# Performance work log

Measured on AMD Instinct MI355X. Metric: run time of the kernel, lower is better.

## Reference

```python
import jax, jax.numpy as jnp
import numpy as np

B, L, F, E, D, N_OUT, FC = 2048, 100, 64, 256, 256, 3, 128


def _lstm_cell(x, h, c, Wi, Wh, b):
    gates = x @ Wi + h @ Wh + b  # (B, 4H)
    i, f, g, o = jnp.split(gates, 4, axis=-1)
    c_new = jax.nn.sigmoid(f) * c + jax.nn.sigmoid(i) * jnp.tanh(g)
    h_new = jax.nn.sigmoid(o) * jnp.tanh(c_new)
    return h_new, c_new


def setup_inputs() -> dict:
    key = jax.random.key(0)
    ks = jax.random.split(key, 12)
    s = 0.05
    return {
        "x": jax.random.normal(ks[0], (B, L, F), jnp.float32),
        # encoder input-attention (shared across timesteps, as in [layer]*look_back)
        "Wa": jax.random.normal(ks[1], (F + E, F), jnp.float32) * s,
        "ba": jnp.zeros((F,), jnp.float32),
        # encoder LSTM cell
        "Wi": jax.random.normal(ks[2], (F, 4 * E), jnp.float32) * s,
        "Wh": jax.random.normal(ks[3], (E, 4 * E), jnp.float32) * s,
        "be": jnp.zeros((4 * E,), jnp.float32),
        # decoder temporal attention
        "Wd": jax.random.normal(ks[4], (E + D, D), jnp.float32) * s,
        "bd": jnp.zeros((D,), jnp.float32),
        "Wl": jax.random.normal(ks[5], (D, 1), jnp.float32) * s,
        "bl": jnp.zeros((1,), jnp.float32),
        # decoder LSTM cell
        "Wdi": jax.random.normal(ks[6], (E, 4 * D), jnp.float32) * s,
        "Wdh": jax.random.normal(ks[7], (D, 4 * D), jnp.float32) * s,
        "bdec": jnp.zeros((4 * D,), jnp.float32),
        # output head: tanh(D->FC) then tanh(FC->1)
        "Wf": jax.random.normal(ks[8], (D, FC), jnp.float32) * s,
        "bf": jnp.zeros((FC,), jnp.float32),
        "Wo": jax.random.normal(ks[9], (FC, 1), jnp.float32) * s,
        "bo": jnp.zeros((1,), jnp.float32),
    }


def reference(x, Wa, ba, Wi, Wh, be, Wd, bd, Wl, bl, Wdi, Wdh, bdec, Wf, bf, Wo, bo):
    # ---------- encoder: per-timestep input attention + LSTM cell ----------
    x_t = jnp.transpose(x, (1, 0, 2))  # (L, B, F)

    def enc_step(carry, xt):
        h, c = carry
        energies = jnp.tanh(jnp.concatenate([xt, h], axis=1) @ Wa + ba)  # (B, F)
        a = jax.nn.softmax(energies, axis=1)
        enc_in = a * xt  # attended input (B, F)
        h, c = _lstm_cell(enc_in, h, c, Wi, Wh, be)
        return (h, c), h

    h0 = jnp.zeros((B, E), x.dtype)
    c0 = jnp.zeros((B, E), x.dtype)
    _, enc_out = jax.lax.scan(enc_step, (h0, c0), x_t)  # (L, B, E)

    # ---------- decoder: temporal attention over encoder states + LSTM ----------
    h_d = jnp.zeros((B, D), x.dtype)
    c_d = jnp.zeros((B, D), x.dtype)
    outs = []
    for _ in range(N_OUT):  # small fixed output horizon
        con = jnp.broadcast_to(h_d[None, :, :], (L, B, D))
        en = jnp.tanh(jnp.concatenate([enc_out, con], axis=2) @ Wd + bd)  # (L, B, D)
        scores = en @ Wl + bl  # (L, B, 1)
        alpha = jax.nn.softmax(scores, axis=0)  # over time
        ctx = jnp.sum(alpha * enc_out, axis=0)  # (B, E)
        h_d, c_d = _lstm_cell(ctx, h_d, c_d, Wdi, Wdh, bdec)
        fc = jnp.tanh(h_d @ Wf + bf)  # (B, FC)
        outs.append(jnp.tanh(fc @ Wo + bo))  # (B, 1)
    return jnp.concatenate(outs, axis=1)  # (B, n_output)
```

## Files before the change

kernel.cpp:

```cpp
#include <hip/hip_runtime.h>
#include <math.h>

#define BB 2048
#define LL 100
#define FF 64
#define EE 256
#define DD 256
#define NOUT 3

#define COMP(v, i) ((i) == 0 ? (v).x : (i) == 1 ? (v).y : (i) == 2 ? (v).z : (v).w)

typedef unsigned short u16;
typedef unsigned int u32;
typedef __attribute__((ext_vector_type(8))) __bf16 bf16x8;
typedef __attribute__((ext_vector_type(4))) float f32x4;
typedef __attribute__((ext_vector_type(2))) float f32x2;

#define MFMA_(A, B, C) __builtin_amdgcn_mfma_f32_16x16x32_bf16((A), (B), (C), 0, 0, 0)

__device__ __forceinline__ float sigmoidf_(float x) {
    return 1.0f / (1.0f + expf(-x));
}
__device__ __forceinline__ float tanhf_(float x) {
    return 1.0f - 2.0f / (1.0f + expf(2.0f * x));
}
__device__ __forceinline__ u16 f2b_(float f) {
    u32 u = __float_as_uint(f);
    u = (u + 0x7FFFu + ((u >> 16) & 1u)) >> 16;
    return (u16)u;
}
__device__ __forceinline__ float b2f_(u16 b) {
    return __uint_as_float(((u32)b) << 16);
}
__device__ __forceinline__ u32 pack2_(float a, float b) {
    return (u32)f2b_(a) | ((u32)f2b_(b) << 16);
}
__device__ __forceinline__ f32x4 splat4(float b) {
    f32x4 v; v[0] = b; v[1] = b; v[2] = b; v[3] = b; return v;
}
__device__ __forceinline__ void split8(const float* v, uint4& H, uint4& L) {
    u16 h[8], lo[8];
    #pragma unroll
    for (int e = 0; e < 8; ++e) {
        h[e]  = f2b_(v[e]);
        lo[e] = f2b_(v[e] - b2f_(h[e]));
    }
    H = make_uint4((u32)h[0]  | ((u32)h[1]  << 16), (u32)h[2]  | ((u32)h[3]  << 16),
                   (u32)h[4]  | ((u32)h[5]  << 16), (u32)h[6]  | ((u32)h[7]  << 16));
    L = make_uint4((u32)lo[0] | ((u32)lo[1] << 16), (u32)lo[2] | ((u32)lo[3] << 16),
                   (u32)lo[4] | ((u32)lo[5] << 16), (u32)lo[6] | ((u32)lo[7] << 16));
}

#define AF(mt, kt, p, ln) (((((mt) * 10 + (kt)) * 2 + (p)) * 64 + (ln)) * 8)

__global__ __launch_bounds__(64) void w_prep(
    const float* __restrict__ Wi, const float* __restrict__ Wh,
    const float* __restrict__ Wa, u16* __restrict__ wp)
{
    const int bid = blockIdx.x;
    const int l   = threadIdx.x;
    const int isA = (bid >= 640);
    const int b2  = isA ? bid - 640 : bid;
    const int nt  = b2 / 10, kt = b2 - nt * 10;
    const int col = nt * 16 + (l & 15);

    float v[8];
    #pragma unroll
    for (int e = 0; e < 8; ++e) {
        const int k = kt * 32 + ((l >> 4) << 3) + e;
        v[e] = isA ? Wa[(size_t)k * 64 + col]
                   : (k < 64 ? Wi[(size_t)k * 1024 + col]
                             : Wh[(size_t)(k - 64) * 1024 + col]);
    }
    uint4 H, L;
    split8(v, H, L);
    *(uint4*)&wp[(size_t)bid * 1024 + (size_t)l * 8]       = H;
    *(uint4*)&wp[(size_t)bid * 1024 + 512 + (size_t)l * 8] = L;
}

__global__ __launch_bounds__(1024) void enc_mfma4(
    const float* __restrict__ x,
    const float* __restrict__ ba, const float* __restrict__ be,
    const u16* __restrict__ wp,
    float* __restrict__ enc_out,
    float* __restrict__ hbuf,
    u32* __restrict__ flags)
{
    __shared__ u16   aFrag[20480];
    __shared__ float x_s[32 * 68];
    __shared__ float e_s[32 * 68];
    __shared__ float gate_s[4][32][64];

    const int bid = blockIdx.x;
    const int g   = (bid & 7) | ((bid >> 5) << 3);
    const int p   = (bid >> 3) & 3;
    const int row0 = g * 32;
    const int tid = threadIdx.x;
    const int l   = tid & 63;
    const int w   = tid >> 6;

    for (int v = tid; v < 20480 / 2; v += 1024) ((u32*)aFrag)[v] = 0u;

    const int ntW = (w >> 2) * 16 + p * 4 + (w & 3);
    uint4 BhR[10];
    #pragma unroll
    for (int kt = 0; kt < 10; ++kt)
        BhR[kt] = *(const uint4*)&wp[(size_t)(ntW * 10 + kt) * 1024 + (size_t)l * 8];

    const float be_r = be[(size_t)ntW * 16 + (l & 15)];
    const float ba_r = (w < 8) ? ba[(w & 3) * 16 + (l & 15)] : 0.f;

    float c_state[2] = {0.f, 0.f};

    __syncthreads();

    for (int t = 0; t < LL; ++t) {
        if (t > 0) {
            if (tid == 0) {
                const u32 target = 4u * (u32)t;
                int guard = 0;
                while (__hip_atomic_load(&flags[g], __ATOMIC_RELAXED,
                                         __HIP_MEMORY_SCOPE_AGENT) < target) {
                    __builtin_amdgcn_s_sleep(1);
                    if (++guard > 2000000) break;
                }
            }
            __syncthreads();
        }

        if (tid < 256) {
            const int kt2 = tid >> 7;
            const int mt  = (tid >> 6) & 1;
            const int l2  = tid & 63;
            const int row2 = mt * 16 + (l2 & 15);
            const int f0   = kt2 * 32 + ((l2 >> 4) << 3);
            const float* xp = x + (size_t)(row0 + row2) * (LL * FF) + (size_t)t * FF + f0;
            float4 xa = *(const float4*)xp;
            float4 xb = *(const float4*)(xp + 4);
            float v[8] = {xa.x, xa.y, xa.z, xa.w, xb.x, xb.y, xb.z, xb.w};
            uint4 H, L;
            split8(v, H, L);
            *(uint4*)&aFrag[AF(mt, kt2, 0, l2)] = H;
            *(uint4*)&aFrag[AF(mt, kt2, 1, l2)] = L;
            *(float4*)&x_s[row2 * 68 + f0]     = xa;
            *(float4*)&x_s[row2 * 68 + f0 + 4] = xb;
        } else if (t > 0) {
            const int v   = tid - 256;
            const int prl = v >> 8;
            const int vv  = v & 255;
            const int row = vv >> 3;
            const int i8  = vv & 7;
            const int ugp = (p + 1 + prl) & 3;
            const int u8  = ugp * 64 + i8 * 8;
            const float* hp_g = hbuf + ((size_t)((t - 1) & 1) * BB + row0 + row) * 256 + u8;
            f32x4 a4, b4;
            asm volatile("global_load_dwordx4 %0, %2, off sc0 sc1\n\t"
                         "global_load_dwordx4 %1, %3, off sc0 sc1\n\t"
                         "s_waitcnt vmcnt(0)"
                         : "=v"(a4), "=v"(b4)
                         : "v"(hp_g), "v"(hp_g + 4) : "memory");
            float v8[8] = {a4[0], a4[1], a4[2], a4[3], b4[0], b4[1], b4[2], b4[3]};
            uint4 H, L;
            split8(v8, H, L);
            const int mt = row >> 4, rowT = row & 15;
            const int kt_h = 2 + (u8 >> 5);
            const int g2   = (u8 & 31) >> 3;
            const int ln   = rowT + (g2 << 4);
            *(uint4*)&aFrag[AF(mt, kt_h, 0, ln)] = H;
            *(uint4*)&aFrag[AF(mt, kt_h, 1, ln)] = L;
        }
        __syncthreads();

        if (w < 8) {
            const int mt  = w >> 2;
            const int nta = w & 3;
            f32x4 ea = splat4(ba_r);
            #pragma unroll
            for (int kt = 0; kt < 10; ++kt) {
                bf16x8 Ah = *(const bf16x8*)&aFrag[AF(mt, kt, 0, l)];
                bf16x8 Al = *(const bf16x8*)&aFrag[AF(mt, kt, 1, l)];
                const size_t o = (size_t)(640 + nta * 10 + kt) * 1024 + (size_t)l * 8;
                bf16x8 Bh = *(const bf16x8*)&wp[o];
                bf16x8 Bl = *(const bf16x8*)&wp[o + 512];
                ea = MFMA_(Ah, Bh, ea);
                ea = MFMA_(Al, Bh, ea);
                ea = MFMA_(Ah, Bl, ea);
            }
            const int colA = nta * 16 + (l & 15);
            #pragma unroll
            for (int r = 0; r < 4; ++r) {
                const int rowT = ((l >> 4) << 2) + r;
                e_s[(mt * 16 + rowT) * 68 + colA] = tanhf_(ea[r]);
            }
        }
        __syncthreads();

        if (tid < 512) {
            const int row2 = tid >> 4;
            const int c4   = (tid & 15) * 4;
            float4 ev = *(const float4*)&e_s[row2 * 68 + c4];
            float m = fmaxf(fmaxf(ev.x, ev.y), fmaxf(ev.z, ev.w));
            #pragma unroll
            for (int msk = 8; msk >= 1; msk >>= 1) m = fmaxf(m, __shfl_xor(m, msk, 64));
            float4 ex;
            ex.x = expf(ev.x - m); ex.y = expf(ev.y - m);
            ex.z = expf(ev.z - m); ex.w = expf(ev.w - m);
            float s = ex.x + ex.y + ex.z + ex.w;
            #pragma unroll
            for (int msk = 8; msk >= 1; msk >>= 1) s += __shfl_xor(s, msk, 64);
            const float inv = 1.f / s;
            float4 xv = *(const float4*)&x_s[row2 * 68 + c4];
            float ein[4] = { ex.x * inv * xv.x, ex.y * inv * xv.y,
                             ex.z * inv * xv.z, ex.w * inv * xv.w };
            const int mt   = row2 >> 4;
            const int rowT = row2 & 15;
            const int kt   = c4 >> 5;
            const int g2   = (c4 & 31) >> 3;
            const int e0   = c4 & 7;
            const int ln   = rowT + (g2 << 4);
            ushort4 h4, l4;
            #pragma unroll
            for (int e = 0; e < 4; ++e) {
                u16 hh = f2b_(ein[e]);
                u16 ll = f2b_(ein[e] - b2f_(hh));
                if (e == 0) { h4.x = hh; l4.x = ll; } else if (e == 1) { h4.y = hh; l4.y = ll; }
                else if (e == 2) { h4.z = hh; l4.z = ll; } else { h4.w = hh; l4.w = ll; }
            }
            *(ushort4*)&aFrag[AF(mt, kt, 0, ln) + e0] = h4;
            *(ushort4*)&aFrag[AF(mt, kt, 1, ln) + e0] = l4;
        }
        __syncthreads();

        f32x4 acc0 = splat4(be_r), acc1 = splat4(be_r);
        #pragma unroll
        for (int kt = 0; kt < 10; ++kt) {
            bf16x8 Ah0 = *(const bf16x8*)&aFrag[AF(0, kt, 0, l)];
            bf16x8 Al0 = *(const bf16x8*)&aFrag[AF(0, kt, 1, l)];
            bf16x8 Ah1 = *(const bf16x8*)&aFrag[AF(1, kt, 0, l)];
            bf16x8 Al1 = *(const bf16x8*)&aFrag[AF(1, kt, 1, l)];
            bf16x8 Bl  = *(const bf16x8*)&wp[(size_t)(ntW * 10 + kt) * 1024 + 512 + (size_t)l * 8];
            bf16x8 Bh  = __builtin_bit_cast(bf16x8, BhR[kt]);
            acc0 = MFMA_(Ah0, Bh, acc0);
            acc1 = MFMA_(Ah1, Bh, acc1);
            acc0 = MFMA_(Al0, Bh, acc0);
            acc1 = MFMA_(Al1, Bh, acc1);
            acc0 = MFMA_(Ah0, Bl, acc0);
            acc1 = MFMA_(Ah1, Bl, acc1);
        }
        {
            const int gate = w >> 2;
            const int ulb  = (w & 3) * 16 + (l & 15);
            #pragma unroll
            for (int r = 0; r < 4; ++r) {
                const int rT = ((l >> 4) << 2) + r;
                gate_s[gate][rT][ulb]      = acc0[r];
                gate_s[gate][16 + rT][ulb] = acc1[r];
            }
        }
        __syncthreads();

        {
            const int row = tid >> 5;
            const int q2  = (tid & 31) * 2;
            float gi0 = gate_s[0][row][q2], gi1 = gate_s[0][row][q2 + 1];
            float gf0 = gate_s[1][row][q2], gf1 = gate_s[1][row][q2 + 1];
            float gg0 = gate_s[2][row][q2], gg1 = gate_s[2][row][q2 + 1];
            float go0 = gate_s[3][row][q2], go1 = gate_s[3][row][q2 + 1];
            float cv0 = sigmoidf_(gf0) * c_state[0] + sigmoidf_(gi0) * tanhf_(gg0);
            float cv1 = sigmoidf_(gf1) * c_state[1] + sigmoidf_(gi1) * tanhf_(gg1);
            c_state[0] = cv0; c_state[1] = cv1;
            float hv0 = sigmoidf_(go0) * tanhf_(cv0);
            float hv1 = sigmoidf_(go1) * tanhf_(cv1);
            const int u_g = p * 64 + q2;
            *(float2*)&enc_out[((size_t)t * BB + row0 + row) * 256 + u_g]
                = make_float2(hv0, hv1);
            float* hp_g = hbuf + ((size_t)(t & 1) * BB + row0 + row) * 256 + u_g;
            f32x2 hv2; hv2[0] = hv0; hv2[1] = hv1;
            asm volatile("global_store_dwordx2 %0, %1, off sc0 sc1"
                         :: "v"(hp_g), "v"(hv2) : "memory");
            const int mt = row >> 4, rowT = row & 15;
            const int kt_h = 2 + (u_g >> 5);
            const int g2   = (u_g & 31) >> 3;
            const int ln   = rowT + (g2 << 4);
            const int e    = u_g & 7;
            ((u32*)aFrag)[(AF(mt, kt_h, 0, ln) + e) >> 1] = pack2_(hv0, hv1);
            u16 h0 = f2b_(hv0), h1 = f2b_(hv1);
            ((u32*)aFrag)[(AF(mt, kt_h, 1, ln) + e) >> 1] =
                (u32)f2b_(hv0 - b2f_(h0)) | ((u32)f2b_(hv1 - b2f_(h1)) << 16);
        }
        asm volatile("s_waitcnt vmcnt(0)" ::: "memory");
        __syncthreads();
        if (tid == 0)
            __hip_atomic_fetch_add(&flags[g], 1u, __ATOMIC_RELEASE,
                                   __HIP_MEMORY_SCOPE_AGENT);
    }
}

__global__ __launch_bounds__(256) void gemm_nk256(
    const float* __restrict__ A, const float* __restrict__ W,
    const float* __restrict__ bias, float* __restrict__ C, int skip_gemm)
{
    __shared__ float a_s[32 * 256];
    const int m0   = blockIdx.x * 32;
    const int tid  = threadIdx.x;
    const int lane = tid & 63;
    const int rg   = tid >> 6;
    const int n0   = lane * 4;

    float4 bias4 = make_float4(0.f, 0.f, 0.f, 0.f);
    if (bias) bias4 = *(const float4*)&bias[n0];

    if (skip_gemm) {
        #pragma unroll
        for (int r = 0; r < 8; ++r)
            *(float4*)&C[(size_t)(m0 + rg * 8 + r) * 256 + n0] = bias4;
        return;
    }

    for (int v = tid; v < 32 * 64; v += 256)
        ((float4*)a_s)[v] = ((const float4*)(A + (size_t)m0 * 256))[v];
    __syncthreads();

    float4 acc[8];
    #pragma unroll
    for (int r = 0; r < 8; ++r) acc[r] = bias4;

    #pragma unroll 2
    for (int k = 0; k < 256; k += 4) {
        float4 wv[4];
        #pragma unroll
        for (int kk = 0; kk < 4; ++kk)
            wv[kk] = *(const float4*)&W[(size_t)(k + kk) * 256 + n0];
        float4 av[8];
        #pragma unroll
        for (int r = 0; r < 8; ++r)
            av[r] = *(const float4*)&a_s[(rg * 8 + r) * 256 + k];
        #pragma unroll
        for (int kk = 0; kk < 4; ++kk) {
            #pragma unroll
            for (int r = 0; r < 8; ++r) {
                float e = COMP(av[r], kk);
                acc[r].x += e * wv[kk].x; acc[r].y += e * wv[kk].y;
                acc[r].z += e * wv[kk].z; acc[r].w += e * wv[kk].w;
            }
        }
    }
    #pragma unroll
    for (int r = 0; r < 8; ++r)
        *(float4*)&C[(size_t)(m0 + rg * 8 + r) * 256 + n0] = acc[r];
}

__global__ __launch_bounds__(256) void pack_ep(
    float* A, const float* __restrict__ W, u16* epOut, int packed)
{
    __shared__ float a_s[32 * 256];
    const int m0   = blockIdx.x * 32;
    const int tid  = threadIdx.x;
    const int lane = tid & 63;
    const int rg   = tid >> 6;
    const int n0   = lane * 4;

    for (int v = tid; v < 32 * 64; v += 256)
        ((float4*)a_s)[v] = ((const float4*)(A + (size_t)m0 * 256))[v];
    __syncthreads();

    float4 acc[8];
    #pragma unroll
    for (int r = 0; r < 8; ++r) acc[r] = make_float4(0.f, 0.f, 0.f, 0.f);

    #pragma unroll 2
    for (int k = 0; k < 256; k += 4) {
        float4 wv[4];
        #pragma unroll
        for (int kk = 0; kk < 4; ++kk)
            wv[kk] = *(const float4*)&W[(size_t)(k + kk) * 256 + n0];
        float4 av[8];
        #pragma unroll
        for (int r = 0; r < 8; ++r)
            av[r] = *(const float4*)&a_s[(rg * 8 + r) * 256 + k];
        #pragma unroll
        for (int kk = 0; kk < 4; ++kk) {
            #pragma unroll
            for (int r = 0; r < 8; ++r) {
                float e = COMP(av[r], kk);
                acc[r].x += e * wv[kk].x; acc[r].y += e * wv[kk].y;
                acc[r].z += e * wv[kk].z; acc[r].w += e * wv[kk].w;
            }
        }
    }

    u16* epu = packed ? (u16*)A : epOut;
    #pragma unroll
    for (int r = 0; r < 8; ++r) {
        const size_t row = (size_t)(m0 + rg * 8 + r);
        ushort4 o;
        o.x = f2b_(acc[r].x); o.y = f2b_(acc[r].y);
        o.z = f2b_(acc[r].z); o.w = f2b_(acc[r].w);
        u16* dst = packed ? (epu + row * 512 + 256 + n0)
                          : (epu + row * 256 + n0);
        *(ushort4*)dst = o;
    }

    if (packed) {
        u32* ab = (u32*)A;
        for (int v = tid; v < 32 * 128; v += 256) {
            const int row = v >> 7, j = v & 127;
            float2 f = *(const float2*)&a_s[(row << 8) + (j << 1)];
            ab[((size_t)(m0 + row)) * 256 + j] = pack2_(f.x, f.y);
        }
    }
}

__global__ __launch_bounds__(256) void scores_ep_f32(
    const float* __restrict__ ep, const float* __restrict__ hp,
    const float* __restrict__ Wl, float* __restrict__ scores)
{
    __shared__ float hp_s[8 * 256];
    const int b0  = blockIdx.x * 8;
    const int l0  = blockIdx.y * 20;
    const int tid = threadIdx.x;
    const int r   = tid >> 5;
    const int g   = tid & 31;

    for (int v = tid; v < 512; v += 256)
        ((float4*)hp_s)[v] = ((const float4*)(hp + (size_t)b0 * 256))[v];
    __syncthreads();

    const float4 wl0 = *(const float4*)&Wl[g * 4];
    const float4 wl1 = *(const float4*)&Wl[128 + g * 4];
    const float4 h0  = *(const float4*)&hp_s[r * 256 + g * 4];
    const float4 h1  = *(const float4*)&hp_s[r * 256 + 128 + g * 4];
    const float* eb  = ep + (size_t)l0 * (BB * 256) + (size_t)(b0 + r) * 256;

    #pragma unroll 2
    for (int li = 0; li < 20; ++li) {
        float4 e0 = *(const float4*)&eb[(size_t)li * (BB * 256) + g * 4];
        float4 e1 = *(const float4*)&eb[(size_t)li * (BB * 256) + 128 + g * 4];
        float p = tanhf_(e0.x + h0.x) * wl0.x + tanhf_(e0.y + h0.y) * wl0.y
                + tanhf_(e0.z + h0.z) * wl0.z + tanhf_(e0.w + h0.w) * wl0.w
                + tanhf_(e1.x + h1.x) * wl1.x + tanhf_(e1.y + h1.y) * wl1.y
                + tanhf_(e1.z + h1.z) * wl1.z + tanhf_(e1.w + h1.w) * wl1.w;
        #pragma unroll
        for (int msk = 16; msk >= 1; msk >>= 1) p += __shfl_xor(p, msk, 64);
        if (g == 0) scores[(size_t)(l0 + li) * BB + b0 + r] = p;
    }
}

__global__ __launch_bounds__(256) void scores_ep_b16(
    const u16* __restrict__ ep, const float* __restrict__ hp,
    const float* __restrict__ Wl, float* __restrict__ scores,
    int sstr, int soff)
{
    __shared__ float hp_s[8 * 256];
    const int b0  = blockIdx.x * 8;
    const int l0  = blockIdx.y * 20;
    const int tid = threadIdx.x;
    const int r   = tid >> 5;
    const int g   = tid & 31;

    for (int v = tid; v < 512; v += 256)
        ((float4*)hp_s)[v] = ((const float4*)(hp + (size_t)b0 * 256))[v];
    __syncthreads();

    const float4 wl0 = *(const float4*)&Wl[g * 4];
    const float4 wl1 = *(const float4*)&Wl[128 + g * 4];
    const float4 h0  = *(const float4*)&hp_s[r * 256 + g * 4];
    const float4 h1  = *(const float4*)&hp_s[r * 256 + 128 + g * 4];

    #pragma unroll 2
    for (int li = 0; li < 20; ++li) {
        const u16* er = ep + ((size_t)(l0 + li) * BB + b0 + r) * sstr + soff;
        ushort4 u0 = *(const ushort4*)&er[g * 4];
        ushort4 u1 = *(const ushort4*)&er[128 + g * 4];
        float p = tanhf_(b2f_(u0.x) + h0.x) * wl0.x + tanhf_(b2f_(u0.y) + h0.y) * wl0.y
                + tanhf_(b2f_(u0.z) + h0.z) * wl0.z + tanhf_(b2f_(u0.w) + h0.w) * wl0.w
                + tanhf_(b2f_(u1.x) + h1.x) * wl1.x + tanhf_(b2f_(u1.y) + h1.y) * wl1.y
                + tanhf_(b2f_(u1.z) + h1.z) * wl1.z + tanhf_(b2f_(u1.w) + h1.w) * wl1.w;
        #pragma unroll
        for (int msk = 16; msk >= 1; msk >>= 1) p += __shfl_xor(p, msk, 64);
        if (g == 0) scores[(size_t)(l0 + li) * BB + b0 + r] = p;
    }
}

__global__ __launch_bounds__(256) void softmax_ctx(
    const float* __restrict__ scores, const float* __restrict__ enc_out,
    float* __restrict__ ctx)
{
    __shared__ float al_s[8 * 100];
    const int b0  = blockIdx.x * 8;
    const int tid = threadIdx.x;
    for (int v = tid; v < 800; v += 256) {
        int r = v / 100, l = v - r * 100;
        al_s[r * 100 + l] = scores[(size_t)l * BB + b0 + r];
    }
    __syncthreads();
    if (tid < 8) {
        float m = -1e30f;
        for (int l = 0; l < LL; ++l) m = fmaxf(m, al_s[tid * 100 + l]);
        float s = 0.f;
        for (int l = 0; l < LL; ++l) { float e = expf(al_s[tid * 100 + l] - m); al_s[tid * 100 + l] = e; s += e; }
        float inv = 1.f / s;
        for (int l = 0; l < LL; ++l) al_s[tid * 100 + l] *= inv;
    }
    __syncthreads();
    float acc[8] = {};
    for (int l = 0; l < LL; ++l) {
        const float* er = enc_out + (size_t)l * (BB * 256) + (size_t)b0 * 256 + tid;
        #pragma unroll
        for (int r = 0; r < 8; ++r) acc[r] += al_s[r * 100 + l] * er[r * 256];
    }
    for (int r = 0; r < 8; ++r) ctx[(size_t)(b0 + r) * 256 + tid] = acc[r];
}

__global__ __launch_bounds__(256) void softmax_ctx_b16(
    const float* __restrict__ scores, const u16* __restrict__ encp,
    float* __restrict__ ctx)
{
    __shared__ float al_s[8 * 100];
    const int b0  = blockIdx.x * 8;
    const int tid = threadIdx.x;
    for (int v = tid; v < 800; v += 256) {
        int r = v / 100, l = v - r * 100;
        al_s[r * 100 + l] = scores[(size_t)l * BB + b0 + r];
    }
    __syncthreads();
    if (tid < 8) {
        float m = -1e30f;
        for (int l = 0; l < LL; ++l) m = fmaxf(m, al_s[tid * 100 + l]);
        float s = 0.f;
        for (int l = 0; l < LL; ++l) { float e = expf(al_s[tid * 100 + l] - m); al_s[tid * 100 + l] = e; s += e; }
        float inv = 1.f / s;
        for (int l = 0; l < LL; ++l) al_s[tid * 100 + l] *= inv;
    }
    __syncthreads();
    float acc[8] = {};
    for (int l = 0; l < LL; ++l) {
        const u16* er = encp + ((size_t)l * BB + b0) * 512 + tid;
        #pragma unroll
        for (int r = 0; r < 8; ++r) acc[r] += al_s[r * 100 + l] * b2f_(er[r * 512]);
    }
    for (int r = 0; r < 8; ++r) ctx[(size_t)(b0 + r) * 256 + tid] = acc[r];
}

__global__ __launch_bounds__(512) void dec_step(
    const float* __restrict__ ctxp,
    const float* __restrict__ Wdi, const float* __restrict__ Wdh,
    const float* __restrict__ bdec,
    float* __restrict__ hd, float* __restrict__ c_st, int first)
{
    __shared__ float ct_s[8 * 256];
    __shared__ float hd_s[8 * 256];
    __shared__ float gate_s[2][8 * 1024];
    const int row0 = blockIdx.x * 8;
    const int tid  = threadIdx.x;
    const int lane = tid & 63, w = tid >> 6;
    const int half = tid >> 8;
    const int ct   = tid & 255;
    const int c0   = ct * 4;

    ((float4*)ct_s)[tid] = ((const float4*)(ctxp + (size_t)row0 * 256))[tid];
    if (!first)
        ((float4*)hd_s)[tid] = ((const float4*)(hd + (size_t)row0 * 256))[tid];
    __syncthreads();

    float4 acc[8];
    {
        float4 b4 = *(const float4*)&bdec[c0];
        float4 bias4 = (half == 0) ? b4 : make_float4(0.f, 0.f, 0.f, 0.f);
        #pragma unroll
        for (int r = 0; r < 8; ++r) acc[r] = bias4;
    }
    if (half == 0) {
        const float* wP = Wdi + c0;
        #pragma unroll 2
        for (int ch = 0; ch < 64; ++ch) {
            const int k0 = ch * 4;
            float4 w0 = *(const float4*)&wP[(size_t)(k0 + 0) * 1024];
            float4 w1 = *(const float4*)&wP[(size_t)(k0 + 1) * 1024];
            float4 w2 = *(const float4*)&wP[(size_t)(k0 + 2) * 1024];
            float4 w3 = *(const float4*)&wP[(size_t)(k0 + 3) * 1024];
            #pragma unroll
            for (int r = 0; r < 8; ++r) {
                float4 av = *(const float4*)&ct_s[r * 256 + k0];
                acc[r].x += av.x * w0.x; acc[r].y += av.x * w0.y;
                acc[r].z += av.x * w0.z; acc[r].w += av.x * w0.w;
                acc[r].x += av.y * w1.x; acc[r].y += av.y * w1.y;
                acc[r].z += av.y * w1.z; acc[r].w += av.y * w1.w;
                acc[r].x += av.z * w2.x; acc[r].y += av.z * w2.y;
                acc[r].z += av.z * w2.z; acc[r].w += av.z * w2.w;
                acc[r].x += av.w * w3.x; acc[r].y += av.w * w3.y;
                acc[r].z += av.w * w3.z; acc[r].w += av.w * w3.w;
            }
        }
    } else if (!first) {
        const float* wP = Wdh + c0;
        #pragma unroll 2
        for (int ch = 0; ch < 64; ++ch) {
            const int k0 = ch * 4;
            float4 w0 = *(const float4*)&wP[(size_t)(k0 + 0) * 1024];
            float4 w1 = *(const float4*)&wP[(size_t)(k0 + 1) * 1024];
            float4 w2 = *(const float4*)&wP[(size_t)(k0 + 2) * 1024];
            float4 w3 = *(const float4*)&wP[(size_t)(k0 + 3) * 1024];
            #pragma unroll
            for (int r = 0; r < 8; ++r) {
                float4 av = *(const float4*)&hd_s[r * 256 + k0];
                acc[r].x += av.x * w0.x; acc[r].y += av.x * w0.y;
                acc[r].z += av.x * w0.z; acc[r].w += av.x * w0.w;
                acc[r].x += av.y * w1.x; acc[r].y += av.y * w1.y;
                acc[r].z += av.y * w1.z; acc[r].w += av.y * w1.w;
                acc[r].x += av.z * w2.x; acc[r].y += av.z * w2.y;
                acc[r].z += av.z * w2.z; acc[r].w += av.z * w2.w;
                acc[r].x += av.w * w3.x; acc[r].y += av.w * w3.y;
                acc[r].z += av.w * w3.z; acc[r].w += av.w * w3.w;
            }
        }
    }
    #pragma unroll
    for (int r = 0; r < 8; ++r)
        *(float4*)&gate_s[half][r * 1024 + c0] = acc[r];
    __syncthreads();

    {
        const float* g0 = &gate_s[0][w * 1024 + lane * 4];
        const float* g1 = &gate_s[1][w * 1024 + lane * 4];
        float4 giA = *(const float4*)&g0[0],   giB = *(const float4*)&g1[0];
        float4 gfA = *(const float4*)&g0[256], gfB = *(const float4*)&g1[256];
        float4 ggA = *(const float4*)&g0[512], ggB = *(const float4*)&g1[512];
        float4 goA = *(const float4*)&g0[768], goB = *(const float4*)&g1[768];
        size_t ci = (size_t)(row0 + w) * 256 + lane * 4;
        float4 c4 = first ? make_float4(0.f, 0.f, 0.f, 0.f)
                          : *(const float4*)&c_st[ci];
        float cc[4] = { c4.x, c4.y, c4.z, c4.w };
        float gi[4] = { giA.x + giB.x, giA.y + giB.y, giA.z + giB.z, giA.w + giB.w };
        float gf[4] = { gfA.x + gfB.x, gfA.y + gfB.y, gfA.z + gfB.z, gfA.w + gfB.w };
        float gg[4] = { ggA.x + ggB.x, ggA.y + ggB.y, ggA.z + ggB.z, ggA.w + ggB.w };
        float go[4] = { goA.x + goB.x, goA.y + goB.y, goA.z + goB.z, goA.w + goB.w };
        float4 cn, hn;
        #pragma unroll
        for (int uu = 0; uu < 4; ++uu) {
            float cv = sigmoidf_(gf[uu]) * cc[uu] + sigmoidf_(gi[uu]) * tanhf_(gg[uu]);
            float hv = sigmoidf_(go[uu]) * tanhf_(cv);
            if (uu == 0) { cn.x = cv; hn.x = hv; } else if (uu == 1) { cn.y = cv; hn.y = hv; }
            else if (uu == 2) { cn.z = cv; hn.z = hv; } else { cn.w = cv; hn.w = hv; }
        }
        *(float4*)&c_st[ci] = cn;
        *(float4*)&hd[ci]   = hn;
    }
}

__global__ __launch_bounds__(256) void head_k(
    const float* __restrict__ hd, const float* __restrict__ Wf,
    const float* __restrict__ bf, const float* __restrict__ Wo,
    const float* __restrict__ bo, float* __restrict__ out, int step)
{
    __shared__ float hd_s[16 * 256];
    __shared__ float fc_s[16 * 128];
    const int b0  = blockIdx.x * 16;
    const int tid = threadIdx.x;
    {
        const float4* hg = (const float4*)(hd + (size_t)b0 * 256);
        for (int i = tid; i < 1024; i += 256) ((float4*)hd_s)[i] = hg[i];
    }
    __syncthreads();
    {
        const int f = tid & 127, rg = tid >> 7;
        float acc[8];
        float bfv = bf[f];
        #pragma unroll
        for (int rr = 0; rr < 8; ++rr) acc[rr] = bfv;
        const float* wp = Wf + f;
        #pragma unroll 2
        for (int k = 0; k < 256; ++k) {
            float wv = wp[k * 128];
            #pragma unroll
            for (int rr = 0; rr < 8; ++rr) acc[rr] += hd_s[(rg * 8 + rr) * 256 + k] * wv;
        }
        for (int rr = 0; rr < 8; ++rr) fc_s[(rg * 8 + rr) * 128 + f] = tanhf_(acc[rr]);
    }
    __syncthreads();
    {
        const int lane = tid & 63, w = tid >> 6;
        const float bov = bo[0];
        #pragma unroll
        for (int rr = 0; rr < 4; ++rr) {
            int r = w * 4 + rr;
            float p = fc_s[r * 128 + lane] * Wo[lane] + fc_s[r * 128 + 64 + lane] * Wo[64 + lane];
            #pragma unroll
            for (int msk = 32; msk >= 1; msk >>= 1) p += __shfl_xor(p, msk, 64);
            if (lane == 0) out[(size_t)(b0 + r) * NOUT + step] = tanhf_(p + bov);
        }
    }
}

extern "C" void kernel_launch(void* const* d_in, const int* in_sizes, int n_in,
                              void* d_out, int out_size, void* d_ws, size_t ws_size,
                              hipStream_t stream)
{
    const float* x    = (const float*)d_in[0];
    const float* Wa   = (const float*)d_in[1];
    const float* ba   = (const float*)d_in[2];
    const float* Wi   = (const float*)d_in[3];
    const float* Wh   = (const float*)d_in[4];
    const float* be   = (const float*)d_in[5];
    const float* Wd   = (const float*)d_in[6];
    const float* bd   = (const float*)d_in[7];
    const float* Wl   = (const float*)d_in[8];
    const float* bl   = (const float*)d_in[9];
    const float* Wdi  = (const float*)d_in[10];
    const float* Wdh  = (const float*)d_in[11];
    const float* bdec = (const float*)d_in[12];
    const float* Wf   = (const float*)d_in[13];
    const float* bf   = (const float*)d_in[14];
    const float* Wo   = (const float*)d_in[15];
    const float* bo   = (const float*)d_in[16];
    float* out = (float*)d_out;

    const size_t f_enc    = (size_t)LL * BB * EE;
    const size_t f_state  = (size_t)BB * EE;
    const size_t f_scores = (size_t)LL * BB;
    const size_t need3 = (f_enc + 3 * f_state + f_scores) * sizeof(float);
    const size_t need2 = need3 + f_enc * sizeof(u16);
    const size_t need1 = need3 + f_enc * sizeof(float);

    float* ws      = (float*)d_ws;
    float* enc_out = ws;
    float* hd      = enc_out + f_enc;
    float* c_d     = hd + f_state;
    float* ctx     = c_d + f_state;
    float* scores  = ctx + f_state;
    float* ep32    = scores + f_scores;
    u16*   ep16    = (u16*)(scores + f_scores);
    float* hp      = ctx;
    u16*   wprep   = (u16*)ctx;
    float* hbuf    = hd;
    u32*   flags   = (u32*)scores;

    if (ws_size < need3) return;
    const int tier = (ws_size >= need1) ? 1 : (ws_size >= need2) ? 2 : 3;

    hipMemsetAsync(flags, 0, 256, stream);
    w_prep<<<680, 64, 0, stream>>>(Wi, Wh, Wa, wprep);
    enc_mfma4<<<256, 1024, 0, stream>>>(x, ba, be, wprep, enc_out, hbuf, flags);

    if (tier == 1)
        gemm_nk256<<<(LL * BB) / 32, 256, 0, stream>>>(
            enc_out, Wd, (const float*)nullptr, ep32, 0);
    else
        pack_ep<<<(LL * BB) / 32, 256, 0, stream>>>(
            enc_out, Wd, ep16, tier == 3 ? 1 : 0);

    for (int s = 0; s < NOUT; ++s) {
        gemm_nk256<<<BB / 32, 256, 0, stream>>>(
            hd, Wd + 256 * 256, bd, hp, s == 0);
        if (tier == 1)
            scores_ep_f32<<<dim3(BB / 8, 5), 256, 0, stream>>>(ep32, hp, Wl, scores);
        else if (tier == 2)
            scores_ep_b16<<<dim3(BB / 8, 5), 256, 0, stream>>>(ep16, hp, Wl, scores, 256, 0);
        else
            scores_ep_b16<<<dim3(BB / 8, 5), 256, 0, stream>>>(
                (const u16*)enc_out, hp, Wl, scores, 512, 256);
        if (tier == 3)
            softmax_ctx_b16<<<BB / 8, 256, 0, stream>>>(scores, (const u16*)enc_out, ctx);
        else
            softmax_ctx<<<BB / 8, 256, 0, stream>>>(scores, enc_out, ctx);
        dec_step<<<BB / 8, 512, 0, stream>>>(ctx, Wdi, Wdh, bdec, hd, c_d, s == 0);
        head_k<<<BB / 16, 256, 0, stream>>>(hd, Wf, bf, Wo, bo, out, s);
    }
}
```

Measured before the change: 2.382 ms.

## Use split-bf16 MFMA for enc_out projection GEMM and tweak encoder sync/registers

```diff
diff --git a/kernel.cpp b/kernel.cpp
--- a/kernel.cpp
+++ b/kernel.cpp
@@ -52,6 +52,7 @@
 }
 
 #define AF(mt, kt, p, ln) (((((mt) * 10 + (kt)) * 2 + (p)) * 64 + (ln)) * 8)
+#define AF2(mt, kt, p, ln) (((((mt) * 8 + (kt)) * 2 + (p)) * 64 + (ln)) * 8)
 
 __global__ __launch_bounds__(64) void w_prep(
     const float* __restrict__ Wi, const float* __restrict__ Wh,
@@ -76,6 +77,26 @@
     split8(v, H, L);
     *(uint4*)&wp[(size_t)bid * 1024 + (size_t)l * 8]       = H;
     *(uint4*)&wp[(size_t)bid * 1024 + 512 + (size_t)l * 8] = L;
+}
+
+__global__ __launch_bounds__(64) void w_prep2(
+    const float* __restrict__ Wd, u16* __restrict__ wp)
+{
+    const int bid = blockIdx.x;
+    const int l   = threadIdx.x;
+    const int nt  = bid >> 3, kt = bid & 7;
+    const int col = nt * 16 + (l & 15);
+    float v[8];
+    #pragma unroll
+    for (int e = 0; e < 8; ++e) {
+        const int k = kt * 32 + ((l >> 4) << 3) + e;
+        v[e] = Wd[(size_t)k * 256 + col];
+    }
+    uint4 H, L;
+    split8(v, H, L);
+    u16* tp = wp + (size_t)(680 + bid) * 1024;
+    *(uint4*)&tp[(size_t)l * 8]       = H;
+    *(uint4*)&tp[512 + (size_t)l * 8] = L;
 }
 
 __global__ __launch_bounds__(1024) void enc_mfma4(
@@ -89,7 +110,7 @@
     __shared__ u16   aFrag[20480];
     __shared__ float x_s[32 * 68];
     __shared__ float e_s[32 * 68];
-    __shared__ float gate_s[4][32][64];
+    __shared__ float gate_s[4][32][66];
 
     const int bid = blockIdx.x;
     const int g   = (bid & 7) | ((bid >> 5) << 3);
@@ -102,10 +123,12 @@
     for (int v = tid; v < 20480 / 2; v += 1024) ((u32*)aFrag)[v] = 0u;
 
     const int ntW = (w >> 2) * 16 + p * 4 + (w & 3);
-    uint4 BhR[10];
-    #pragma unroll
-    for (int kt = 0; kt < 10; ++kt)
+    uint4 BhR[10], BlR[10];
+    #pragma unroll
+    for (int kt = 0; kt < 10; ++kt) {
         BhR[kt] = *(const uint4*)&wp[(size_t)(ntW * 10 + kt) * 1024 + (size_t)l * 8];
+        BlR[kt] = *(const uint4*)&wp[(size_t)(ntW * 10 + kt) * 1024 + 512 + (size_t)l * 8];
+    }
 
     const float be_r = be[(size_t)ntW * 16 + (l & 15)];
     const float ba_r = (w < 8) ? ba[(w & 3) * 16 + (l & 15)] : 0.f;
@@ -115,19 +138,6 @@
     __syncthreads();
 
     for (int t = 0; t < LL; ++t) {
-        if (t > 0) {
-            if (tid == 0) {
-                const u32 target = 4u * (u32)t;
-                int guard = 0;
-                while (__hip_atomic_load(&flags[g], __ATOMIC_RELAXED,
-                                         __HIP_MEMORY_SCOPE_AGENT) < target) {
-                    __builtin_amdgcn_s_sleep(1);
-                    if (++guard > 2000000) break;
-                }
-            }
-            __syncthreads();
-        }
-
         if (tid < 256) {
             const int kt2 = tid >> 7;
             const int mt  = (tid >> 6) & 1;
@@ -145,6 +155,13 @@
             *(float4*)&x_s[row2 * 68 + f0]     = xa;
             *(float4*)&x_s[row2 * 68 + f0 + 4] = xb;
         } else if (t > 0) {
+            const u32 target = 4u * (u32)t;
+            int guard = 0;
+            while (__hip_atomic_load(&flags[g * 32], __ATOMIC_RELAXED,
+                                     __HIP_MEMORY_SCOPE_AGENT) < target) {
+                __builtin_amdgcn_s_sleep(1);
+                if (++guard > 4000000) break;
+            }
             const int v   = tid - 256;
             const int prl = v >> 8;
             const int vv  = v & 255;
@@ -238,8 +255,8 @@
             bf16x8 Al0 = *(const bf16x8*)&aFrag[AF(0, kt, 1, l)];
             bf16x8 Ah1 = *(const bf16x8*)&aFrag[AF(1, kt, 0, l)];
             bf16x8 Al1 = *(const bf16x8*)&aFrag[AF(1, kt, 1, l)];
-            bf16x8 Bl  = *(const bf16x8*)&wp[(size_t)(ntW * 10 + kt) * 1024 + 512 + (size_t)l * 8];
             bf16x8 Bh  = __builtin_bit_cast(bf16x8, BhR[kt]);
+            bf16x8 Bl  = __builtin_bit_cast(bf16x8, BlR[kt]);
             acc0 = MFMA_(Ah0, Bh, acc0);
             acc1 = MFMA_(Ah1, Bh, acc1);
             acc0 = MFMA_(Al0, Bh, acc0);
@@ -291,8 +308,79 @@
         asm volatile("s_waitcnt vmcnt(0)" ::: "memory");
         __syncthreads();
         if (tid == 0)
-            __hip_atomic_fetch_add(&flags[g], 1u, __ATOMIC_RELEASE,
+            __hip_atomic_fetch_add(&flags[g * 32], 1u, __ATOMIC_RELEASE,
                                    __HIP_MEMORY_SCOPE_AGENT);
+    }
+}
+
+__global__ __launch_bounds__(256) void gemm_ep_mfma(
+    const float* __restrict__ A, const u16* __restrict__ wp,
+    float* __restrict__ C)
+{
+    __shared__ u16   aF[2 * 8 * 2 * 64 * 8];
+    __shared__ float c_s[32 * 260];
+    const int m0  = blockIdx.x * 32;
+    const int tid = threadIdx.x;
+    const int l   = tid & 63;
+    const int w   = tid >> 6;
+
+    for (int s = tid; s < 1024; s += 256) {
+        const int mt = s >> 9, kt = (s >> 6) & 7, l2 = s & 63;
+        const int row2 = mt * 16 + (l2 & 15);
+        const int k0   = kt * 32 + ((l2 >> 4) << 3);
+        const float* ap = A + (size_t)(m0 + row2) * 256 + k0;
+        float4 xa = *(const float4*)ap;
+        float4 xb = *(const float4*)(ap + 4);
+        float v[8] = {xa.x, xa.y, xa.z, xa.w, xb.x, xb.y, xb.z, xb.w};
+        uint4 H, L;
+        split8(v, H, L);
+        *(uint4*)&aF[AF2(mt, kt, 0, l2)] = H;
+        *(uint4*)&aF[AF2(mt, kt, 1, l2)] = L;
+    }
+    __syncthreads();
+
+    f32x4 acc[2][4];
+    #pragma unroll
+    for (int mt = 0; mt < 2; ++mt)
+        #pragma unroll
+        for (int j = 0; j < 4; ++j) acc[mt][j] = splat4(0.f);
+
+    #pragma unroll
+    for (int kt = 0; kt < 8; ++kt) {
+        bf16x8 Ah0 = *(const bf16x8*)&aF[AF2(0, kt, 0, l)];
+        bf16x8 Al0 = *(const bf16x8*)&aF[AF2(0, kt, 1, l)];
+        bf16x8 Ah1 = *(const bf16x8*)&aF[AF2(1, kt, 0, l)];
+        bf16x8 Al1 = *(const bf16x8*)&aF[AF2(1, kt, 1, l)];
+        #pragma unroll
+        for (int j = 0; j < 4; ++j) {
+            const int nt = w * 4 + j;
+            const u16* bt = wp + (size_t)(680 + nt * 8 + kt) * 1024 + (size_t)l * 8;
+            bf16x8 Bh = *(const bf16x8*)bt;
+            bf16x8 Bl = *(const bf16x8*)(bt + 512);
+            acc[0][j] = MFMA_(Ah0, Bh, acc[0][j]);
+            acc[1][j] = MFMA_(Ah1, Bh, acc[1][j]);
+            acc[0][j] = MFMA_(Al0, Bh, acc[0][j]);
+            acc[1][j] = MFMA_(Al1, Bh, acc[1][j]);
+            acc[0][j] = MFMA_(Ah0, Bl, acc[0][j]);
+            acc[1][j] = MFMA_(Ah1, Bl, acc[1][j]);
+        }
+    }
+
+    #pragma unroll
+    for (int mt = 0; mt < 2; ++mt)
+        #pragma unroll
+        for (int j = 0; j < 4; ++j) {
+            const int col = (w * 4 + j) * 16 + (l & 15);
+            #pragma unroll
+            for (int r = 0; r < 4; ++r) {
+                const int row = mt * 16 + ((l >> 4) << 2) + r;
+                c_s[row * 260 + col] = acc[mt][j][r];
+            }
+        }
+    __syncthreads();
+    for (int v = tid; v < 32 * 64; v += 256) {
+        const int row = v >> 6, c4 = (v & 63) << 2;
+        *(float4*)&C[(size_t)(m0 + row) * 256 + c4] = *(const float4*)&c_s[row * 260 + c4];
     }
 }
 
@@ -738,13 +826,13 @@
     if (ws_size < need3) return;
     const int tier = (ws_size >= need1) ? 1 : (ws_size >= need2) ? 2 : 3;
 
-    hipMemsetAsync(flags, 0, 256, stream);
+    hipMemsetAsync(flags, 0, 64 * 32 * sizeof(u32), stream);
     w_prep<<<680, 64, 0, stream>>>(Wi, Wh, Wa, wprep);
+    w_prep2<<<128, 64, 0, stream>>>(Wd, wprep);
     enc_mfma4<<<256, 1024, 0, stream>>>(x, ba, be, wprep, enc_out, hbuf, flags);
 
     if (tier == 1)
-        gemm_nk256<<<(LL * BB) / 32, 256, 0, stream>>>(
-            enc_out, Wd, (const float*)nullptr, ep32, 0);
+        gemm_ep_mfma<<<(LL * BB) / 32, 256, 0, stream>>>(enc_out, wprep, ep32);
     else
         pack_ep<<<(LL * BB) / 32, 256, 0, stream>>>(
             enc_out, Wd, ep16, tier == 3 ? 1 : 0);
```

Result: slower. 2.754 ms (+15.6%).
